# Performance work log

Measured on AMD Instinct MI355X. Metric: run time of the kernel, lower is better.

The kernel has to match this reference:

```python
import jax, jax.numpy as jnp
import numpy as np

# Fixed-point emulation: SharedFxpShift = 8 -> scale 256. Integer bit-shifts of the
# original int32/int8 pipeline are emulated in float32 (multiply/divide by 2^8) with
# int8 clamping, keeping the same dataflow (resblock -> pred head -> bin packing ->
# upsample -> (N,8,ch) child scatter) so a quantized kernel can be checked against it.
SHIFT = 256.0

def requant(x):
    # RequantFxpToScaledInt8: shift down and clamp to int8 range
    return jnp.clip(x * (1.0 / SHIFT), -128.0, 127.0)

def prelu(x, a):
    return jnp.where(x >= 0, x, a * x)

def resblock(x, w1, w2, a):
    # SparseResBlockIn32W8Out32: requant -> linear -> prelu -> requant -> linear -> +x
    h = requant(x)
    h = h @ w1.T
    h = prelu(h, a)
    h = requant(h)
    h = h @ w2.T
    return x + h

def setup_inputs() -> dict:
    key = jax.random.key(0)
    ks = jax.random.split(key, 16)
    N, CH = 50000, 256
    w = lambda k, shp: jax.random.normal(k, shp, dtype=jnp.float32) * 0.05
    return {
        'x': jax.random.normal(ks[0], (N, CH), dtype=jnp.float32) * SHIFT,
        'cur_bin': jax.random.randint(ks[1], (N, 8), 0, 2, dtype=jnp.int32),
        'w_dec1': w(ks[2], (CH, CH)),
        'w_dec2': w(ks[3], (CH, CH)),
        'a_dec': jax.random.uniform(ks[4], (1,), dtype=jnp.float32),
        'w_pconv': w(ks[5], (CH, CH)),
        'a_pconv': jax.random.uniform(ks[6], (1,), dtype=jnp.float32),
        'w_plin': w(ks[7], (255, CH)),
        'w_up1': w(ks[8], (CH, CH + 8)),
        'a_up1': jax.random.uniform(ks[9], (1,), dtype=jnp.float32),
        'w_ur1': w(ks[10], (CH, CH)),
        'w_ur2': w(ks[11], (CH, CH)),
        'a_ur': jax.random.uniform(ks[12], (1,), dtype=jnp.float32),
        'w_uout': w(ks[13], (2048, CH)),
    }

def reference(x, cur_bin, w_dec1, w_dec2, a_dec, w_pconv, a_pconv, w_plin,
              w_up1, a_up1, w_ur1, w_ur2, a_ur, w_uout):
    N, CH = x.shape
    binf = cur_bin.astype(jnp.float32)
    # dec: residual block
    rec = resblock(x, w_dec1, w_dec2, a_dec)
    # pred: requant -> conv+prelu -> requant -> linear(ch,255)
    h = requant(rec)
    h = prelu(h @ w_pconv.T, a_pconv)
    h = requant(h)
    cur_pred = h @ w_plin.T                                   # [N, 255]
    # bin -> octree symbol: (cur_bin << arange(8)).sum(1) - 1
    bin2oct = jnp.arange(8, dtype=jnp.int32)
    cur_oct = jnp.sum(cur_bin << bin2oct, axis=1).astype(jnp.int16) - 1  # [N]
    # upsample: cat(rec, bin << shift) -> requant -> lin+prelu -> resblock -> requant -> lin(ch*8)
    u = jnp.concatenate([rec, binf * SHIFT], axis=1)          # [N, CH+8]
    u = requant(u)
    u = prelu(u @ w_up1.T, a_up1)
    u = resblock(u, w_ur1, w_ur2, a_ur)
    u = requant(u)
    u = u @ w_uout.T                                          # [N, 8*CH]
    # child gather: original does reshape(N,8,CH)[cur_bin.bool()] (ragged);
    # we keep the dense [N,8,CH] with unoccupied children zeroed (jit-friendly).
    rec_out = u.reshape(N, 8, CH) * binf[:, :, None]
    return rec_out, cur_pred, cur_oct
```

## Files before the change

### kernel.cpp

```cpp
#include <hip/hip_runtime.h>

typedef __bf16 bf16x8 __attribute__((ext_vector_type(8)));
typedef float  f32x4  __attribute__((ext_vector_type(4)));

#define OFF_DEC1  0
#define OFF_DEC2  65536
#define OFF_PCONV 131072
#define OFF_PLIN  196608
#define OFF_UP1   262144
#define OFF_UR1   335872
#define OFF_UR2   401408
#define OFF_UOUT  466944
#define WB_TOTAL  991232

__device__ __align__(16) unsigned short g_wb[WB_TOTAL];

__device__ __forceinline__ unsigned short f2bf(float f) {
  union { float f; unsigned u; } c; c.f = f;
  unsigned u = c.u + 0x7FFFu + ((c.u >> 16) & 1u);
  return (unsigned short)(u >> 16);
}
__device__ __forceinline__ float bf2f(unsigned short b) {
  union { unsigned u; float f; } c; c.u = ((unsigned)b) << 16;
  return c.f;
}
__device__ __forceinline__ float reqf(float v) {
  return fminf(fmaxf(v * 0.00390625f, -128.f), 127.f);
}

__global__ void wconv_kernel(const float* __restrict__ wd1, const float* __restrict__ wd2,
                             const float* __restrict__ wpc, const float* __restrict__ wpl,
                             const float* __restrict__ wu1, const float* __restrict__ wr1,
                             const float* __restrict__ wr2, const float* __restrict__ wuo) {
  int t = blockIdx.x * 256 + threadIdx.x;
  if (t >= WB_TOTAL) return;
  const float* src; int local, Ksrc = 256, Msrc = 256, rowOff = 0;
  if      (t < OFF_DEC2)  { src = wd1; local = t; }
  else if (t < OFF_PCONV) { src = wd2; local = t - OFF_DEC2; }
  else if (t < OFF_PLIN)  { src = wpc; local = t - OFF_PCONV; }
  else if (t < OFF_UP1)   { src = wpl; local = t - OFF_PLIN; Msrc = 255; }
  else if (t < OFF_UR1)   { src = wu1; local = t - OFF_UP1; Ksrc = 264; }
  else if (t < OFF_UR2)   { src = wr1; local = t - OFF_UR1; }
  else if (t < OFF_UOUT)  { src = wr2; local = t - OFF_UR2; }
  else { local = t - OFF_UOUT; int c = local >> 16; local &= 65535; src = wuo; rowOff = c * 256; }
  const int s = local >> 13, j = local & 8191;
  const int wv = j >> 10, lq = (j >> 8) & 3, mt = (j >> 7) & 1;
  const int l15 = (j >> 3) & 15, kk = j & 7;
  const int m = wv * 32 + mt * 16 + l15;
  const int k = s * 32 + lq * 8 + kk;
  float v = (m < Msrc && k < Ksrc) ? src[(size_t)(rowOff + m) * Ksrc + k] : 0.f;
  g_wb[t] = f2bf(v);
}


__device__ __forceinline__ void zero_acc(f32x4 (&acc)[2][4]) {
#pragma unroll
  for (int i = 0; i < 2; ++i)
#pragma unroll
    for (int j = 0; j < 4; ++j) acc[i][j] = (f32x4){0.f, 0.f, 0.f, 0.f};
}

__device__ __forceinline__ void prelu_acc(f32x4 (&acc)[2][4], float a) {
#pragma unroll
  for (int i = 0; i < 2; ++i)
#pragma unroll
    for (int j = 0; j < 4; ++j)
#pragma unroll
      for (int r = 0; r < 4; ++r) {
        float v = acc[i][j][r];
        acc[i][j][r] = v >= 0.f ? v : a * v;
      }
}

__device__ __forceinline__ void stageW(const unsigned short* __restrict__ src,
                                       unsigned short* dst, int w, int l) {
#pragma unroll
  for (int i = 0; i < 2; ++i) {
    const int off = w * 1024 + i * 512 + l * 8;
    __builtin_amdgcn_global_load_lds(
        (const __attribute__((address_space(1))) unsigned*)(src + off),
        (__attribute__((address_space(3))) unsigned*)(dst + off),
        16, 0, 0);
  }
}

__device__ __forceinline__ void mfma_slice(const unsigned short* wl, const unsigned short* sAct,
                                           int w, int l15, int lq, int kb, f32x4 (&acc)[2][4]) {
  bf16x8 af[4];
#pragma unroll
  for (int nt = 0; nt < 4; ++nt) {
    const int row = nt * 16 + l15;
    af[nt] = *(const bf16x8*)((const char*)sAct + row * 512 + (kb ^ ((row & 7) << 4)));
  }
#pragma unroll
  for (int mt = 0; mt < 2; ++mt) {
    bf16x8 bfr = *(const bf16x8*)(wl + w * 1024 + lq * 256 + mt * 128 + l15 * 8);
#pragma unroll
    for (int nt = 0; nt < 4; ++nt)
      acc[mt][nt] = __builtin_amdgcn_mfma_f32_16x16x32_bf16(bfr, af[nt], acc[mt][nt], 0, 0, 0);
  }
}

template<int NKS, bool BIN_TAIL>
__device__ __forceinline__ void gemm_cnt(const unsigned short* __restrict__ wcur,
                                         const unsigned short* __restrict__ wnext,
                                         unsigned short*& wl, unsigned short*& wn,
                                         const unsigned short* sAct,
                                         const unsigned short* sBinA,
                                         int w, int l, int l15, int lq,
                                         f32x4 (&acc)[2][4]) {
#pragma unroll
  for (int ks = 0; ks < NKS; ++ks) {
    if (ks < NKS - 1) {
      stageW(wcur + (ks + 1) * 8192, wn, w, l);
      asm volatile("s_waitcnt vmcnt(2)" ::: "memory");
    } else if (wnext) {
      stageW(wnext, wn, w, l);
      asm volatile("s_waitcnt vmcnt(2)" ::: "memory");
    } else {
      asm volatile("s_waitcnt vmcnt(0)" ::: "memory");
    }
    __builtin_amdgcn_sched_barrier(0);
    __builtin_amdgcn_s_setprio(1);
    if (BIN_TAIL && ks == NKS - 1) {
      bf16x8 af[4];
#pragma unroll
      for (int nt = 0; nt < 4; ++nt)
        af[nt] = *(const bf16x8*)(sBinA + (nt * 16 + l15) * 32 + lq * 8);
#pragma unroll
      for (int mt = 0; mt < 2; ++mt) {
        bf16x8 bfr = *(const bf16x8*)(wl + w * 1024 + lq * 256 + mt * 128 + l15 * 8);
#pragma unroll
        for (int nt = 0; nt < 4; ++nt)
          acc[mt][nt] = __builtin_amdgcn_mfma_f32_16x16x32_bf16(bfr, af[nt], acc[mt][nt], 0, 0, 0);
      }
    } else {
      mfma_slice(wl, sAct, w, l15, lq, ks * 64 + lq * 16, acc);
    }
    __builtin_amdgcn_s_setprio(0);
    unsigned short* t2 = wl; wl = wn; wn = t2;
  }
}

__device__ __forceinline__ void stage_rq(const f32x4 (&acc)[2][4], unsigned short* dst,
                                         int w, int l15, int lq) {
#pragma unroll
  for (int nt = 0; nt < 4; ++nt) {
    const int row = nt * 16 + l15;
    const int swz = (row & 7) << 4;
#pragma unroll
    for (int mt = 0; mt < 2; ++mt) {
      const int ch2 = (w * 32 + mt * 16 + lq * 4) * 2;
      ushort4 b4;
      b4.x = f2bf(reqf(acc[mt][nt][0]));
      b4.y = f2bf(reqf(acc[mt][nt][1]));
      b4.z = f2bf(reqf(acc[mt][nt][2]));
      b4.w = f2bf(reqf(acc[mt][nt][3]));
      *(ushort4*)((char*)dst + row * 512 + (ch2 ^ swz)) = b4;
    }
  }
}

__global__ __launch_bounds__(512, 4) void fused_kernel(
    const float* __restrict__ x, const int* __restrict__ cur_bin,
    const float* __restrict__ a_dec, const float* __restrict__ a_pconv,
    const float* __restrict__ a_up1, const float* __restrict__ a_ur,
    float* __restrict__ out, int N)
{
  __shared__ __align__(16) unsigned short sA[64 * 256];
  __shared__ __align__(16) unsigned short sW0[8192];
  __shared__ __align__(16) unsigned short sW1[8192];
  __shared__ __align__(16) unsigned short sBinA[64 * 32];

  const int tid = threadIdx.x;
  const int w = tid >> 6, l = tid & 63;
  const int l15 = l & 15, lq = l >> 4;
  const int r0 = blockIdx.x * 64;
  const size_t PRED_BASE = (size_t)N * 2048;
  const size_t OCT_BASE  = PRED_BASE + (size_t)N * 255;

  const float A_DEC = a_dec[0], A_PCONV = a_pconv[0], A_UP1 = a_up1[0], A_UR = a_ur[0];

  unsigned short *wl = sW0, *wn = sW1;
  stageW(g_wb + OFF_DEC1, wl, w, l);

  for (int i = tid; i < 64 * 32; i += 512) {
    const int row = i >> 5, j = i & 31;
    float bv = 0.f;
    if (j < 8 && (r0 + row) < N) bv = (float)cur_bin[(size_t)(r0 + row) * 8 + j];
    sBinA[i] = (j < 8) ? f2bf(bv) : (unsigned short)0;
  }
  if (tid < 64 && (r0 + tid) < N) {
    int s = 0;
#pragma unroll
    for (int j = 0; j < 8; ++j) s += cur_bin[(size_t)(r0 + tid) * 8 + j] << j;
    out[OCT_BASE + r0 + tid] = (float)(s - 1);
  }
#pragma unroll
  for (int it = 0; it < 8; ++it) {
    const int e = it * 2048 + tid * 4;
    const int row = e >> 8, col = e & 255;
    float4 xv = make_float4(0.f, 0.f, 0.f, 0.f);
    if ((r0 + row) < N) xv = *(const float4*)(x + (size_t)(r0 + row) * 256 + col);
    ushort4 b4;
    b4.x = f2bf(reqf(xv.x)); b4.y = f2bf(reqf(xv.y));
    b4.z = f2bf(reqf(xv.z)); b4.w = f2bf(reqf(xv.w));
    *(ushort4*)((char*)sA + row * 512 + ((col * 2) ^ ((row & 7) << 4))) = b4;
  }
  __syncthreads();

  f32x4 acc[2][4];

  zero_acc(acc);
  gemm_cnt<8, false>(g_wb + OFF_DEC1, g_wb + OFF_DEC2, wl, wn, sA, sBinA, w, l, l15, lq, acc);
  prelu_acc(acc, A_DEC);
  __syncthreads();
  stage_rq(acc, sA, w, l15, lq);
  __syncthreads();

  zero_acc(acc);
  gemm_cnt<8, false>(g_wb + OFF_DEC2, g_wb + OFF_UP1, wl, wn, sA, sBinA, w, l, l15, lq, acc);
  __syncthreads();
#pragma unroll
  for (int nt = 0; nt < 4; ++nt) {
    const int row = nt * 16 + l15;
    const int swz = (row & 7) << 4;
#pragma unroll
    for (int mt = 0; mt < 2; ++mt) {
      const int ch0 = w * 32 + mt * 16 + lq * 4;
      float4 xv = make_float4(0.f, 0.f, 0.f, 0.f);
      if ((r0 + row) < N) xv = *(const float4*)(x + (size_t)(r0 + row) * 256 + ch0);
      ushort4 b4;
      b4.x = f2bf(reqf(xv.x + acc[mt][nt][0]));
      b4.y = f2bf(reqf(xv.y + acc[mt][nt][1]));
      b4.z = f2bf(reqf(xv.z + acc[mt][nt][2]));
      b4.w = f2bf(reqf(xv.w + acc[mt][nt][3]));
      *(ushort4*)((char*)sA + row * 512 + ((ch0 * 2) ^ swz)) = b4;
    }
  }
  __syncthreads();

  unsigned u1p[2][4][2];
  zero_acc(acc);
  gemm_cnt<9, true>(g_wb + OFF_UP1, g_wb + OFF_PCONV, wl, wn, sA, sBinA, w, l, l15, lq, acc);
  prelu_acc(acc, A_UP1);
#pragma unroll
  for (int i = 0; i < 2; ++i)
#pragma unroll
    for (int j = 0; j < 4; ++j)
#pragma unroll
      for (int p = 0; p < 2; ++p)
        u1p[i][j][p] = (unsigned)f2bf(acc[i][j][2 * p]) |
                       ((unsigned)f2bf(acc[i][j][2 * p + 1]) << 16);

  zero_acc(acc);
  gemm_cnt<8, false>(g_wb + OFF_PCONV, g_wb + OFF_PLIN, wl, wn, sA, sBinA, w, l, l15, lq, acc);
  prelu_acc(acc, A_PCONV);
  __syncthreads();
  stage_rq(acc, sA, w, l15, lq);
  __syncthreads();

  zero_acc(acc);
  gemm_cnt<8, false>(g_wb + OFF_PLIN, g_wb + OFF_UR1, wl, wn, sA, sBinA, w, l, l15, lq, acc);
#pragma unroll
  for (int nt = 0; nt < 4; ++nt) {
    const int row = nt * 16 + l15;
    if ((r0 + row) < N) {
      float* rp = out + PRED_BASE + (size_t)(r0 + row) * 255;
#pragma unroll
      for (int mt = 0; mt < 2; ++mt) {
        const int col0 = w * 32 + mt * 16 + lq * 4;
#pragma unroll
        for (int r = 0; r < 4; ++r)
          if (col0 + r < 255)
            rp[col0 + r] = acc[mt][nt][r];
      }
    }
  }
  __syncthreads();

#pragma unroll
  for (int nt = 0; nt < 4; ++nt) {
    const int row = nt * 16 + l15;
    const int swz = (row & 7) << 4;
#pragma unroll
    for (int mt = 0; mt < 2; ++mt) {
      const int ch2 = (w * 32 + mt * 16 + lq * 4) * 2;
      ushort4 b4;
      b4.x = f2bf(reqf(bf2f((unsigned short)(u1p[mt][nt][0]))));
      b4.y = f2bf(reqf(bf2f((unsigned short)(u1p[mt][nt][0] >> 16))));
      b4.z = f2bf(reqf(bf2f((unsigned short)(u1p[mt][nt][1]))));
      b4.w = f2bf(reqf(bf2f((unsigned short)(u1p[mt][nt][1] >> 16))));
      *(ushort4*)((char*)sA + row * 512 + (ch2 ^ swz)) = b4;
    }
  }
  __syncthreads();

  zero_acc(acc);
  gemm_cnt<8, false>(g_wb + OFF_UR1, g_wb + OFF_UR2, wl, wn, sA, sBinA, w, l, l15, lq, acc);
  prelu_acc(acc, A_UR);
  __syncthreads();
  stage_rq(acc, sA, w, l15, lq);
  __syncthreads();

  zero_acc(acc);
  gemm_cnt<8, false>(g_wb + OFF_UR2, g_wb + OFF_UOUT, wl, wn, sA, sBinA, w, l, l15, lq, acc);
#pragma unroll
  for (int i = 0; i < 2; ++i)
#pragma unroll
    for (int j = 0; j < 4; ++j) {
      acc[i][j][0] += bf2f((unsigned short)(u1p[i][j][0]));
      acc[i][j][1] += bf2f((unsigned short)(u1p[i][j][0] >> 16));
      acc[i][j][2] += bf2f((unsigned short)(u1p[i][j][1]));
      acc[i][j][3] += bf2f((unsigned short)(u1p[i][j][1] >> 16));
    }
  __syncthreads();
  stage_rq(acc, sA, w, l15, lq);
  __syncthreads();

#pragma unroll 1
  for (int c = 0; c < 8; ++c) {
    zero_acc(acc);
    const unsigned short* wnxt = (c < 7) ? (g_wb + OFF_UOUT + (c + 1) * 65536) : nullptr;
    gemm_cnt<8, false>(g_wb + OFF_UOUT + c * 65536, wnxt, wl, wn, sA, sBinA, w, l, l15, lq, acc);
#pragma unroll
    for (int nt = 0; nt < 4; ++nt) {
      const int row = nt * 16 + l15;
      if ((r0 + row) < N) {
        const float m = sBinA[row * 32 + c] ? 1.f : 0.f;
        float* rp = out + (size_t)(r0 + row) * 2048 + c * 256;
#pragma unroll
        for (int mt = 0; mt < 2; ++mt) {
          const int ch0 = w * 32 + mt * 16 + lq * 4;
          f32x4 v;
          v[0] = acc[mt][nt][0] * m; v[1] = acc[mt][nt][1] * m;
          v[2] = acc[mt][nt][2] * m; v[3] = acc[mt][nt][3] * m;
          *(f32x4*)(rp + ch0) = v;
        }
      }
    }
  }
}

extern "C" void kernel_launch(void* const* d_in, const int* in_sizes, int n_in,
                              void* d_out, int out_size, void* d_ws, size_t ws_size,
                              hipStream_t stream) {
  const float* x        = (const float*)d_in[0];
  const int*   cur_bin  = (const int*)d_in[1];
  const float* w_dec1   = (const float*)d_in[2];
  const float* w_dec2   = (const float*)d_in[3];
  const float* a_dec    = (const float*)d_in[4];
  const float* w_pconv  = (const float*)d_in[5];
  const float* a_pconv  = (const float*)d_in[6];
  const float* w_plin   = (const float*)d_in[7];
  const float* w_up1    = (const float*)d_in[8];
  const float* a_up1    = (const float*)d_in[9];
  const float* w_ur1    = (const float*)d_in[10];
  const float* w_ur2    = (const float*)d_in[11];
  const float* a_ur     = (const float*)d_in[12];
  const float* w_uout   = (const float*)d_in[13];

  const int N = in_sizes[0] / 256;

  wconv_kernel<<<(WB_TOTAL + 255) / 256, 256, 0, stream>>>(
      w_dec1, w_dec2, w_pconv, w_plin, w_up1, w_ur1, w_ur2, w_uout);

  fused_kernel<<<(N + 63) / 64, 512, 0, stream>>>(
      x, cur_bin, a_dec, a_pconv, a_up1, a_ur, (float*)d_out, N);
}
```

Before: 245.8 us.

## Split final uout GEMM into separate kernel parallelized over row tiles and child chunks

The fused kernel now stops after the upsample resblock and writes the requantized bf16 activation to a workspace buffer. A new kernel launches one block per (row tile, child chunk) pair, so the 8 output chunks of the largest GEMM run in parallel across 8x more blocks instead of serially inside one block. Block indices are remapped so that consecutive blocks share the same weight chunk. The cost is an extra global round trip of the intermediate activation, a second launch, and loads of u_g rows past N on the last tile, which depend on the workspace being large enough.

```diff
diff --git a/kernel.cpp b/kernel.cpp
--- a/kernel.cpp
+++ b/kernel.cpp
@@ -161,11 +161,11 @@
   }
 }
 
-__global__ __launch_bounds__(512, 4) void fused_kernel(
+__global__ __launch_bounds__(512, 4) void kernel_a(
     const float* __restrict__ x, const int* __restrict__ cur_bin,
     const float* __restrict__ a_dec, const float* __restrict__ a_pconv,
     const float* __restrict__ a_up1, const float* __restrict__ a_ur,
-    float* __restrict__ out, int N)
+    float* __restrict__ out, unsigned short* __restrict__ u_g, int N)
 {
   __shared__ __align__(16) unsigned short sA[64 * 256];
   __shared__ __align__(16) unsigned short sW0[8192];
@@ -304,7 +304,7 @@
   __syncthreads();
 
   zero_acc(acc);
-  gemm_cnt<8, false>(g_wb + OFF_UR2, g_wb + OFF_UOUT, wl, wn, sA, sBinA, w, l, l15, lq, acc);
+  gemm_cnt<8, false>(g_wb + OFF_UR2, nullptr, wl, wn, sA, sBinA, w, l, l15, lq, acc);
 #pragma unroll
   for (int i = 0; i < 2; ++i)
 #pragma unroll
@@ -314,29 +314,74 @@
       acc[i][j][2] += bf2f((unsigned short)(u1p[i][j][1]));
       acc[i][j][3] += bf2f((unsigned short)(u1p[i][j][1] >> 16));
     }
-  __syncthreads();
-  stage_rq(acc, sA, w, l15, lq);
-  __syncthreads();
-
-#pragma unroll 1
-  for (int c = 0; c < 8; ++c) {
-    zero_acc(acc);
-    const unsigned short* wnxt = (c < 7) ? (g_wb + OFF_UOUT + (c + 1) * 65536) : nullptr;
-    gemm_cnt<8, false>(g_wb + OFF_UOUT + c * 65536, wnxt, wl, wn, sA, sBinA, w, l, l15, lq, acc);
-#pragma unroll
-    for (int nt = 0; nt < 4; ++nt) {
-      const int row = nt * 16 + l15;
-      if ((r0 + row) < N) {
-        const float m = sBinA[row * 32 + c] ? 1.f : 0.f;
-        float* rp = out + (size_t)(r0 + row) * 2048 + c * 256;
-#pragma unroll
-        for (int mt = 0; mt < 2; ++mt) {
-          const int ch0 = w * 32 + mt * 16 + lq * 4;
-          f32x4 v;
-          v[0] = acc[mt][nt][0] * m; v[1] = acc[mt][nt][1] * m;
-          v[2] = acc[mt][nt][2] * m; v[3] = acc[mt][nt][3] * m;
-          *(f32x4*)(rp + ch0) = v;
-        }
+#pragma unroll
+  for (int nt = 0; nt < 4; ++nt) {
+    const int row = nt * 16 + l15;
+    if ((r0 + row) < N) {
+#pragma unroll
+      for (int mt = 0; mt < 2; ++mt) {
+        const int ch0 = w * 32 + mt * 16 + lq * 4;
+        ushort4 b4;
+        b4.x = f2bf(reqf(acc[mt][nt][0]));
+        b4.y = f2bf(reqf(acc[mt][nt][1]));
+        b4.z = f2bf(reqf(acc[mt][nt][2]));
+        b4.w = f2bf(reqf(acc[mt][nt][3]));
+        *(ushort4*)(u_g + (size_t)(r0 + row) * 256 + ch0) = b4;
+      }
+    }
+  }
+}
+
+__global__ __launch_bounds__(512, 4) void uout_kernel(
+    const unsigned short* __restrict__ u_g, const int* __restrict__ cur_bin,
+    float* __restrict__ out, int N, int RT)
+{
+  __shared__ __align__(16) unsigned short sA[64 * 256];
+  __shared__ __align__(16) unsigned short sW0[8192];
+  __shared__ __align__(16) unsigned short sW1[8192];
+  __shared__ float sBin[64];
+
+  const int tid = threadIdx.x;
+  const int w = tid >> 6, l = tid & 63;
+  const int l15 = l & 15, lq = l >> 4;
+
+  const int bid = blockIdx.x;
+  const int wg  = (bid & 7) * RT + (bid >> 3);
+  const int rt  = wg >> 3, c = wg & 7;
+  const int r0  = rt * 64;
+
+  unsigned short *wl = sW0, *wn = sW1;
+  const unsigned short* wsrc = g_wb + OFF_UOUT + c * 65536;
+  stageW(wsrc, wl, w, l);
+
+#pragma unroll
+  for (int it = 0; it < 2; ++it) {
+    const int e = it * 4096 + tid * 8;
+    const int row = e >> 8, col = e & 255;
+    uint4 v = *(const uint4*)(u_g + (size_t)(r0 + row) * 256 + col);
+    *(uint4*)((char*)sA + row * 512 + ((col * 2) ^ ((row & 7) << 4))) = v;
+  }
+  if (tid < 64)
+    sBin[tid] = ((r0 + tid) < N && cur_bin[(size_t)(r0 + tid) * 8 + c]) ? 1.f : 0.f;
+  __syncthreads();
+
+  f32x4 acc[2][4];
+  zero_acc(acc);
+  gemm_cnt<8, false>(wsrc, nullptr, wl, wn, sA, sA, w, l, l15, lq, acc);
+
+#pragma unroll
+  for (int nt = 0; nt < 4; ++nt) {
+    const int row = nt * 16 + l15;
+    if ((r0 + row) < N) {
+      const float m = sBin[row];
+      float* rp = out + (size_t)(r0 + row) * 2048 + c * 256;
+#pragma unroll
+      for (int mt = 0; mt < 2; ++mt) {
+        const int ch0 = w * 32 + mt * 16 + lq * 4;
+        f32x4 v;
+        v[0] = acc[mt][nt][0] * m; v[1] = acc[mt][nt][1] * m;
+        v[2] = acc[mt][nt][2] * m; v[3] = acc[mt][nt][3] * m;
+        *(f32x4*)(rp + ch0) = v;
       }
     }
   }
@@ -360,11 +405,15 @@
   const float* a_ur     = (const float*)d_in[12];
   const float* w_uout   = (const float*)d_in[13];
 
-  const int N = in_sizes[0] / 256;
+  const int N  = in_sizes[0] / 256;
+  const int RT = (N + 63) / 64;
+  unsigned short* u_g = (unsigned short*)d_ws;
 
   wconv_kernel<<<(WB_TOTAL + 255) / 256, 256, 0, stream>>>(
       w_dec1, w_dec2, w_pconv, w_plin, w_up1, w_ur1, w_ur2, w_uout);
 
-  fused_kernel<<<(N + 63) / 64, 512, 0, stream>>>(
-      x, cur_bin, a_dec, a_pconv, a_up1, a_ur, (float*)d_out, N);
-}
+  kernel_a<<<RT, 512, 0, stream>>>(
+      x, cur_bin, a_dec, a_pconv, a_up1, a_ur, (float*)d_out, u_g, N);
+
+  uout_kernel<<<RT * 8, 512, 0, stream>>>(u_g, cur_bin, (float*)d_out, N, RT);
+}
```

New measurement: 258.2 us. 1.05x slower.

## Split weight staging into half-slices to shrink LDS and raise occupancy

Applied to the files above, without the earlier changes.

Reorders packed weight layout so each 32-wide K slice is split into two 16-row halves, staged into 4K-element double buffers one half per step. This reduces shared memory per block and raises launch bounds minimum blocks, aiming to fit more blocks per CU and better hide latency. It doubles the number of staging/wait steps and tightens the register budget, risking spills or more sync overhead.

```diff
diff --git a/kernel.cpp b/kernel.cpp
--- a/kernel.cpp
+++ b/kernel.cpp
@@ -44,9 +44,9 @@
   else if (t < OFF_UOUT)  { src = wr2; local = t - OFF_UR2; }
   else { local = t - OFF_UOUT; int c = local >> 16; local &= 65535; src = wuo; rowOff = c * 256; }
   const int s = local >> 13, j = local & 8191;
-  const int wv = j >> 10, lq = (j >> 8) & 3, mt = (j >> 7) & 1;
+  const int h = j >> 12, wv = (j >> 9) & 7, lq = (j >> 7) & 3;
   const int l15 = (j >> 3) & 15, kk = j & 7;
-  const int m = wv * 32 + mt * 16 + l15;
+  const int m = wv * 32 + h * 16 + l15;
   const int k = s * 32 + lq * 8 + kk;
   float v = (m < Msrc && k < Ksrc) ? src[(size_t)(rowOff + m) * Ksrc + k] : 0.f;
   g_wb[t] = f2bf(v);
@@ -72,33 +72,13 @@
       }
 }
 
-__device__ __forceinline__ void stageW(const unsigned short* __restrict__ src,
-                                       unsigned short* dst, int w, int l) {
-#pragma unroll
-  for (int i = 0; i < 2; ++i) {
-    const int off = w * 1024 + i * 512 + l * 8;
-    __builtin_amdgcn_global_load_lds(
-        (const __attribute__((address_space(1))) unsigned*)(src + off),
-        (__attribute__((address_space(3))) unsigned*)(dst + off),
-        16, 0, 0);
-  }
-}
-
-__device__ __forceinline__ void mfma_slice(const unsigned short* wl, const unsigned short* sAct,
-                                           int w, int l15, int lq, int kb, f32x4 (&acc)[2][4]) {
-  bf16x8 af[4];
-#pragma unroll
-  for (int nt = 0; nt < 4; ++nt) {
-    const int row = nt * 16 + l15;
-    af[nt] = *(const bf16x8*)((const char*)sAct + row * 512 + (kb ^ ((row & 7) << 4)));
-  }
-#pragma unroll
-  for (int mt = 0; mt < 2; ++mt) {
-    bf16x8 bfr = *(const bf16x8*)(wl + w * 1024 + lq * 256 + mt * 128 + l15 * 8);
-#pragma unroll
-    for (int nt = 0; nt < 4; ++nt)
-      acc[mt][nt] = __builtin_amdgcn_mfma_f32_16x16x32_bf16(bfr, af[nt], acc[mt][nt], 0, 0, 0);
-  }
+__device__ __forceinline__ void stageWh(const unsigned short* __restrict__ src,
+                                        unsigned short* dst, int w, int l) {
+  const int off = w * 512 + l * 8;
+  __builtin_amdgcn_global_load_lds(
+      (const __attribute__((address_space(1))) unsigned*)(src + off),
+      (__attribute__((address_space(3))) unsigned*)(dst + off),
+      16, 0, 0);
 }
 
 template<int NKS, bool BIN_TAIL>
@@ -109,34 +89,37 @@
                                          const unsigned short* sBinA,
                                          int w, int l, int l15, int lq,
                                          f32x4 (&acc)[2][4]) {
-#pragma unroll
-  for (int ks = 0; ks < NKS; ++ks) {
-    if (ks < NKS - 1) {
-      stageW(wcur + (ks + 1) * 8192, wn, w, l);
-      asm volatile("s_waitcnt vmcnt(2)" ::: "memory");
-    } else if (wnext) {
-      stageW(wnext, wn, w, l);
-      asm volatile("s_waitcnt vmcnt(2)" ::: "memory");
+  bf16x8 af[4];
+#pragma unroll
+  for (int hs = 0; hs < 2 * NKS; ++hs) {
+    const int ks = hs >> 1, mt = hs & 1;
+    const unsigned short* nsrc = (hs < 2 * NKS - 1) ? (wcur + (hs + 1) * 4096) : wnext;
+    if (nsrc) {
+      stageWh(nsrc, wn, w, l);
+      asm volatile("s_waitcnt vmcnt(1)" ::: "memory");
     } else {
       asm volatile("s_waitcnt vmcnt(0)" ::: "memory");
     }
     __builtin_amdgcn_sched_barrier(0);
     __builtin_amdgcn_s_setprio(1);
-    if (BIN_TAIL && ks == NKS - 1) {
-      bf16x8 af[4];
-#pragma unroll
-      for (int nt = 0; nt < 4; ++nt)
-        af[nt] = *(const bf16x8*)(sBinA + (nt * 16 + l15) * 32 + lq * 8);
-#pragma unroll
-      for (int mt = 0; mt < 2; ++mt) {
-        bf16x8 bfr = *(const bf16x8*)(wl + w * 1024 + lq * 256 + mt * 128 + l15 * 8);
+    if (mt == 0) {
+      if (BIN_TAIL && ks == NKS - 1) {
 #pragma unroll
         for (int nt = 0; nt < 4; ++nt)
-          acc[mt][nt] = __builtin_amdgcn_mfma_f32_16x16x32_bf16(bfr, af[nt], acc[mt][nt], 0, 0, 0);
+          af[nt] = *(const bf16x8*)(sBinA + (nt * 16 + l15) * 32 + lq * 8);
+      } else {
+        const int kb = ks * 64 + lq * 16;
+#pragma unroll
+        for (int nt = 0; nt < 4; ++nt) {
+          const int row = nt * 16 + l15;
+          af[nt] = *(const bf16x8*)((const char*)sAct + row * 512 + (kb ^ ((row & 7) << 4)));
+        }
       }
-    } else {
-      mfma_slice(wl, sAct, w, l15, lq, ks * 64 + lq * 16, acc);
-    }
+    }
+    bf16x8 bfr = *(const bf16x8*)(wl + w * 512 + lq * 128 + l15 * 8);
+#pragma unroll
+    for (int nt = 0; nt < 4; ++nt)
+      acc[mt][nt] = __builtin_amdgcn_mfma_f32_16x16x32_bf16(bfr, af[nt], acc[mt][nt], 0, 0, 0);
     __builtin_amdgcn_s_setprio(0);
     unsigned short* t2 = wl; wl = wn; wn = t2;
   }
@@ -161,15 +144,15 @@
   }
 }
 
-__global__ __launch_bounds__(512, 4) void fused_kernel(
+__global__ __launch_bounds__(512, 6) void fused_kernel(
     const float* __restrict__ x, const int* __restrict__ cur_bin,
     const float* __restrict__ a_dec, const float* __restrict__ a_pconv,
     const float* __restrict__ a_up1, const float* __restrict__ a_ur,
     float* __restrict__ out, int N)
 {
   __shared__ __align__(16) unsigned short sA[64 * 256];
-  __shared__ __align__(16) unsigned short sW0[8192];
-  __shared__ __align__(16) unsigned short sW1[8192];
+  __shared__ __align__(16) unsigned short sW0[4096];
+  __shared__ __align__(16) unsigned short sW1[4096];
   __shared__ __align__(16) unsigned short sBinA[64 * 32];
 
   const int tid = threadIdx.x;
@@ -182,7 +165,7 @@
   const float A_DEC = a_dec[0], A_PCONV = a_pconv[0], A_UP1 = a_up1[0], A_UR = a_ur[0];
 
   unsigned short *wl = sW0, *wn = sW1;
-  stageW(g_wb + OFF_DEC1, wl, w, l);
+  stageWh(g_wb + OFF_DEC1, wl, w, l);
 
   for (int i = tid; i < 64 * 32; i += 512) {
     const int row = i >> 5, j = i & 31;
```

Measured after the change: 372.6 us. 1.52x slower.
